# Optimization experiments

Measured on AMD Instinct MI355X. Metric: run time of the kernel, lower is better.

Reference implementation:

```python
import jax, jax.numpy as jnp
import numpy as np

N = 50000      # nodes
T = 24         # sequence length
D_IN = 16      # lstm input dim
H = 64         # lstm hidden dim
SD = 9         # static feature dim
G_IN, G_HID, G_OUT = 64, 64, 1
E = 1600000    # edges
NUM_GRAPHS = 500


def setup_inputs() -> dict:
    key = jax.random.key(0)
    ks = jax.random.split(key, 16)
    s = 0.1
    return {
        "x": jax.random.normal(ks[0], (N, T, D_IN), dtype=jnp.float32),
        "sdi": jax.random.normal(ks[1], (N, SD), dtype=jnp.float32),
        "edge_index": jax.random.randint(ks[2], (2, E), 0, N, dtype=jnp.int64),
        "batch": jnp.sort(jax.random.randint(ks[3], (N,), 0, NUM_GRAPHS, dtype=jnp.int64)),
        # LSTM params (torch gate order: i, f, g, o)
        "W_ih": s * jax.random.normal(ks[4], (4 * H, D_IN), dtype=jnp.float32),
        "W_hh": s * jax.random.normal(ks[5], (4 * H, H), dtype=jnp.float32),
        "b_ih": s * jax.random.normal(ks[6], (4 * H,), dtype=jnp.float32),
        "b_hh": s * jax.random.normal(ks[7], (4 * H,), dtype=jnp.float32),
        # Linear l1: (hidden + static) -> graph_input
        "l1_W": s * jax.random.normal(ks[8], (G_IN, H + SD), dtype=jnp.float32),
        "l1_b": s * jax.random.normal(ks[9], (G_IN,), dtype=jnp.float32),
        # GCNConv layers (weight stored [out, in] like torch Linear)
        "gcn1_W": s * jax.random.normal(ks[10], (G_HID, G_IN), dtype=jnp.float32),
        "gcn1_b": s * jax.random.normal(ks[11], (G_HID,), dtype=jnp.float32),
        "gcn2_W": s * jax.random.normal(ks[12], (G_OUT, G_HID), dtype=jnp.float32),
        "gcn2_b": s * jax.random.normal(ks[13], (G_OUT,), dtype=jnp.float32),
    }


def _lstm_last_hidden(x, W_ih, W_hh, b_ih, b_hh):
    # x: [N, T, D]; returns final hidden state h_T: [N, H]
    xg = jnp.einsum("ntd,gd->tng", x, W_ih) + (b_ih + b_hh)  # [T, N, 4H]
    h0 = jnp.zeros((x.shape[0], H), x.dtype)
    c0 = jnp.zeros((x.shape[0], H), x.dtype)

    def step(carry, g_t):
        h, c = carry
        g = g_t + h @ W_hh.T
        i, f, gg, o = jnp.split(g, 4, axis=-1)
        i = jax.nn.sigmoid(i)
        f = jax.nn.sigmoid(f)
        gg = jnp.tanh(gg)
        o = jax.nn.sigmoid(o)
        c = f * c + i * gg
        h = o * jnp.tanh(c)
        return (h, c), None

    (h, _), _ = jax.lax.scan(step, (h0, c0), xg)
    return h


def _gcn_conv(x, edge_index, W, b):
    # PyG GCNConv: add self-loops, symmetric normalization, scatter-add at dst.
    n = x.shape[0]
    loop = jnp.arange(n, dtype=edge_index.dtype)
    row = jnp.concatenate([edge_index[0], loop])  # src
    col = jnp.concatenate([edge_index[1], loop])  # dst
    deg = jax.ops.segment_sum(jnp.ones_like(col, dtype=x.dtype), col, num_segments=n)
    dis = jnp.where(deg > 0, jax.lax.rsqrt(jnp.maximum(deg, 1.0)), 0.0)
    norm = dis[row] * dis[col]                    # [E + N]
    h = x @ W.T                                   # [N, out]
    msg = h[row] * norm[:, None]                  # gather + scale
    out = jax.ops.segment_sum(msg, col, num_segments=n)
    return out + b


def reference(x, sdi, edge_index, batch, W_ih, W_hh, b_ih, b_hh,
              l1_W, l1_b, gcn1_W, gcn1_b, gcn2_W, gcn2_b):
    h = _lstm_last_hidden(x, W_ih, W_hh, b_ih, b_hh)       # [N, H]
    z = jnp.concatenate([h, sdi], axis=-1) @ l1_W.T + l1_b  # [N, G_IN]
    z = jax.nn.relu(_gcn_conv(z, edge_index, gcn1_W, gcn1_b))
    z = _gcn_conv(z, edge_index, gcn2_W, gcn2_b)            # [N, 1]
    # global mean pool over graph ids
    sums = jax.ops.segment_sum(z, batch, num_segments=NUM_GRAPHS)
    cnts = jax.ops.segment_sum(jnp.ones((z.shape[0],), z.dtype), batch, num_segments=NUM_GRAPHS)
    pooled = sums / jnp.maximum(cnts, 1.0)[:, None]         # [G, 1]
    return pooled.reshape(-1)
```

## Files before the change

### kernel.cpp

```cpp
#include <hip/hip_runtime.h>
#include <hip/hip_bf16.h>

#define N_NODES 50000
#define T_SEQ 24
#define D_IN 16
#define H_DIM 64
#define SD 9
#define E_EDGES 1600000
#define NUM_GRAPHS 500
#define NBLK 196

typedef _Float16 half8 __attribute__((ext_vector_type(8)));
typedef _Float16 half4 __attribute__((ext_vector_type(4)));
typedef float floatx4 __attribute__((ext_vector_type(4)));

__device__ __forceinline__ float fsig(float x) {
    return __fdividef(1.0f, 1.0f + __expf(-x));
}
__device__ __forceinline__ float ftanh(float x) {
    return 1.0f - __fdividef(2.0f, 1.0f + __expf(2.0f * x));
}

__global__ __launch_bounds__(256, 2) void lstm_mfma(
    const float* __restrict__ x,
    const float* __restrict__ W_ih, const float* __restrict__ W_hh,
    const float* __restrict__ b_ih, const float* __restrict__ b_hh,
    float* __restrict__ hout)
{
    __shared__ _Float16 smem[2048 + 24 * 16 * 16];
    _Float16* hb0 = smem;
    _Float16* hb1 = smem + 1024;
    _Float16* xbuf = smem + 2048;

    const int tid  = threadIdx.x;
    const int lane = tid & 63;
    const int w    = tid >> 6;
    const int lr   = lane & 15;
    const int lg   = lane >> 4;
    const int nbase = blockIdx.x * 16;

    half8 bw[4][3];
    float bias[4];
#pragma unroll
    for (int ct = 0; ct < 4; ct++) {
        const int r = ct * 64 + w * 16 + lr;
        bias[ct] = b_ih[r] + b_hh[r];
#pragma unroll
        for (int kt = 0; kt < 2; kt++) {
            const float* p = W_hh + r * 64 + kt * 32 + 8 * lg;
            half8 f;
#pragma unroll
            for (int e = 0; e < 8; e++) f[e] = (_Float16)p[e];
            bw[ct][kt] = f;
        }
        half8 f = {(_Float16)0, (_Float16)0, (_Float16)0, (_Float16)0,
                   (_Float16)0, (_Float16)0, (_Float16)0, (_Float16)0};
        if (lg < 2) {
            const float* p = W_ih + r * 16 + 8 * lg;
#pragma unroll
            for (int e = 0; e < 8; e++) f[e] = (_Float16)p[e];
        }
        bw[ct][2] = f;
    }

#pragma unroll
    for (int it = 0; it < 6; it++) {
        const int f4 = tid + it * 256;
        const int fi = f4 * 4;
        const int n  = fi / 384;
        const int rem = fi - n * 384;
        const int t  = rem >> 4;
        const int d  = rem & 15;
        const float4 v = *reinterpret_cast<const float4*>(
            x + (size_t)(nbase + n) * 384 + rem);
        half4 hv = {(_Float16)v.x, (_Float16)v.y, (_Float16)v.z, (_Float16)v.w};
        *reinterpret_cast<half4*>(&xbuf[t * 256 + n * 16 + d]) = hv;
    }
    if (tid < 128) { ((int*)hb0)[tid] = 0; ((int*)hb0)[tid + 128] = 0; ((int*)hb0)[tid + 256] = 0; ((int*)hb0)[tid + 384] = 0; }

    const int u = w * 16 + lr;
    int ra[2];
#pragma unroll
    for (int kt = 0; kt < 2; kt++)
        ra[kt] = lr * 64 + 8 * ((4 * kt + lg) ^ (lr & 7));
    int woff[4];
#pragma unroll
    for (int j = 0; j < 4; j++) {
        const int nj = 4 * lg + j;
        woff[j] = nj * 64 + (u & 7) + 8 * ((u >> 3) ^ (nj & 7));
    }
    const int xro = lr * 16 + 8 * (lg & 1);

    float c_reg[4];
#pragma unroll
    for (int j = 0; j < 4; j++) c_reg[j] = 0.0f;

    __syncthreads();

    auto step = [&](int tl, bool last, _Float16* hR, _Float16* hW) {
        floatx4 acc[4];
#pragma unroll
        for (int ct = 0; ct < 4; ct++) {
            floatx4 a = {bias[ct], bias[ct], bias[ct], bias[ct]};
            acc[ct] = a;
        }
        const half8 ax = *reinterpret_cast<const half8*>(&xbuf[tl * 256 + xro]);
        const half8 ah0 = *reinterpret_cast<const half8*>(&hR[ra[0]]);
        const half8 ah1 = *reinterpret_cast<const half8*>(&hR[ra[1]]);
#pragma unroll
        for (int ct = 0; ct < 4; ct++)
            acc[ct] = __builtin_amdgcn_mfma_f32_16x16x32_f16(ah0, bw[ct][0], acc[ct], 0, 0, 0);
#pragma unroll
        for (int ct = 0; ct < 4; ct++)
            acc[ct] = __builtin_amdgcn_mfma_f32_16x16x32_f16(ah1, bw[ct][1], acc[ct], 0, 0, 0);
#pragma unroll
        for (int ct = 0; ct < 4; ct++)
            acc[ct] = __builtin_amdgcn_mfma_f32_16x16x32_f16(ax, bw[ct][2], acc[ct], 0, 0, 0);

#pragma unroll
        for (int j = 0; j < 4; j++) {
            const float ig = fsig(acc[0][j]);
            const float fg = fsig(acc[1][j]);
            const float gg = ftanh(acc[2][j]);
            const float og = fsig(acc[3][j]);
            const float cv = fg * c_reg[j] + ig * gg;
            c_reg[j] = cv;
            const float hv = og * ftanh(cv);
            hW[woff[j]] = (_Float16)hv;
            if (last) {
                const int gn = nbase + 4 * lg + j;
                hout[(size_t)gn * H_DIM + u] = hv;
            }
        }
        __syncthreads();
    };

    for (int tb = 0; tb < 6; tb++) {
        const int t0 = tb * 4;
        step(t0 + 0, false, hb0, hb1);
        step(t0 + 1, false, hb1, hb0);
        step(t0 + 2, false, hb0, hb1);
        step(t0 + 3, tb == 5, hb1, hb0);
    }
}

__global__ void count_deg(const int* __restrict__ ei, int* __restrict__ cnt) {
    int e = blockIdx.x * 256 + threadIdx.x;
    if (e < E_EDGES) {
        int c = ei[E_EDGES + e];
        if ((unsigned)c < N_NODES) atomicAdd(&cnt[c], 1);
    }
}

__global__ __launch_bounds__(256) void scanA(const int* __restrict__ cnt,
                                             int* __restrict__ ptr,
                                             float* __restrict__ dis,
                                             int* __restrict__ bsum)
{
    __shared__ int wsum[4];
    const int tid = threadIdx.x, lane = tid & 63, wv = tid >> 6;
    const int i = blockIdx.x * 256 + tid;
    const int orig = (i < N_NODES) ? cnt[i] : 0;
    int v = orig;
#pragma unroll
    for (int d = 1; d < 64; d <<= 1) {
        int nb = __shfl_up(v, d, 64);
        if (lane >= d) v += nb;
    }
    if (lane == 63) wsum[wv] = v;
    __syncthreads();
    int woff = 0;
#pragma unroll
    for (int k = 0; k < 3; k++) if (k < wv) woff += wsum[k];
    if (i < N_NODES) {
        ptr[i] = woff + v - orig;
        dis[i] = rsqrtf((float)(orig + 1));
    }
    if (tid == 255) bsum[blockIdx.x] = woff + v;
}

__global__ __launch_bounds__(256) void scanB(const int* __restrict__ bsum,
                                             int* __restrict__ boff,
                                             int* __restrict__ ptr)
{
    __shared__ int wsum[4];
    const int tid = threadIdx.x, lane = tid & 63, wv = tid >> 6;
    const int orig = (tid < NBLK) ? bsum[tid] : 0;
    int v = orig;
#pragma unroll
    for (int d = 1; d < 64; d <<= 1) {
        int nb = __shfl_up(v, d, 64);
        if (lane >= d) v += nb;
    }
    if (lane == 63) wsum[wv] = v;
    __syncthreads();
    int woff = 0;
#pragma unroll
    for (int k = 0; k < 3; k++) if (k < wv) woff += wsum[k];
    if (tid < NBLK) boff[tid] = woff + v - orig;
    if (tid == 255) ptr[N_NODES] = woff + v;
}

__global__ __launch_bounds__(256) void scanC(int* __restrict__ ptr,
                                             const int* __restrict__ boff,
                                             int* __restrict__ cursor)
{
    const int i = blockIdx.x * 256 + threadIdx.x;
    if (i < N_NODES) {
        const int p = ptr[i] + boff[blockIdx.x];
        ptr[i] = p;
        cursor[i] = p;
    }
}

__global__ void fill_csr(const int* __restrict__ ei, int* __restrict__ cursor,
                         int* __restrict__ csr)
{
    int e = blockIdx.x * 256 + threadIdx.x;
    if (e < E_EDGES) {
        int r = ei[e];
        int c = ei[E_EDGES + e];
        if ((unsigned)r < N_NODES && (unsigned)c < N_NODES) {
            int slot = atomicAdd(&cursor[c], 1);
            csr[slot] = r;
        }
    }
}

__global__ void combine_w(const float* __restrict__ g1W, const float* __restrict__ l1W,
                          const float* __restrict__ l1b,
                          float* __restrict__ Wc, float* __restrict__ bc)
{
    int idx = blockIdx.x * 256 + threadIdx.x;
    int o = idx / 74, j = idx - o * 74;
    if (o >= 64) return;
    float acc = 0.0f;
    if (j < 73) {
#pragma unroll 8
        for (int k = 0; k < 64; k++) acc += g1W[o * 64 + k] * l1W[k * 73 + j];
        Wc[o * 73 + j] = acc;
    } else {
#pragma unroll 8
        for (int k = 0; k < 64; k++) acc += g1W[o * 64 + k] * l1b[k];
        bc[o] = acc;
    }
}

__global__ __launch_bounds__(256) void xform1(
    const float* __restrict__ h, const float* __restrict__ sdi,
    const float* __restrict__ Wc, const float* __restrict__ bc,
    const float* __restrict__ dis, float* __restrict__ m)
{
    __shared__ float wlds[64 * 73];
    __shared__ float blds[64];
    __shared__ float row[4][80];
    for (int i = threadIdx.x; i < 64 * 73; i += 256) wlds[i] = Wc[i];
    if (threadIdx.x < 64) blds[threadIdx.x] = bc[threadIdx.x];
    __syncthreads();
    const int wv = threadIdx.x >> 6, o = threadIdx.x & 63;
    for (int n = blockIdx.x * 4 + wv; n < N_NODES; n += gridDim.x * 4) {
        row[wv][o] = h[(size_t)n * 64 + o];
        if (o < SD) row[wv][64 + o] = sdi[(size_t)n * SD + o];
        __builtin_amdgcn_wave_barrier();
        float acc = blds[o];
#pragma unroll 8
        for (int j = 0; j < 73; j++) acc += wlds[o * 73 + j] * row[wv][j];
        __builtin_amdgcn_wave_barrier();
        m[(size_t)n * 64 + o] = acc * dis[n];
    }
}

__global__ __launch_bounds__(256) void gatherfin1s2(
    const int* __restrict__ ptr, const int* __restrict__ csr,
    const float* __restrict__ m, const float* __restrict__ dis,
    const float* __restrict__ b1, const float* __restrict__ W2,
    float* __restrict__ s2)
{
    const int wid = (blockIdx.x * 256 + threadIdx.x) >> 6;
    const int f = threadIdx.x & 63;
    if (wid >= N_NODES) return;
    const int b = ptr[wid];
    const int e = ptr[wid + 1];
    float a0 = 0.0f, a1 = 0.0f, a2 = 0.0f, a3 = 0.0f;
    int i = b;
    for (; i + 4 <= e; i += 4) {
        const int s0 = csr[i], s1 = csr[i + 1], sc2 = csr[i + 2], s3 = csr[i + 3];
        a0 += m[(size_t)s0 * 64 + f];
        a1 += m[(size_t)s1 * 64 + f];
        a2 += m[(size_t)sc2 * 64 + f];
        a3 += m[(size_t)s3 * 64 + f];
    }
    for (; i < e; i++) a0 += m[(size_t)csr[i] * 64 + f];
    const float self = m[(size_t)wid * 64 + f];
    const float dn = dis[wid];
    const float v = dn * (((a0 + a1) + (a2 + a3)) + self) + b1[f];
    const float z1 = v > 0.0f ? v : 0.0f;
    float p = z1 * W2[f];
#pragma unroll
    for (int off = 32; off >= 1; off >>= 1) p += __shfl_xor(p, off, 64);
    if (f == 0) s2[wid] = dn * p;
}

__global__ void gather2fin(const int* __restrict__ ptr, const int* __restrict__ csr,
                           const float* __restrict__ s2, const float* __restrict__ dis,
                           const float* __restrict__ b2, const int* __restrict__ batch,
                           float* __restrict__ gsum, float* __restrict__ gcnt)
{
    int n = blockIdx.x * 256 + threadIdx.x;
    if (n >= N_NODES) return;
    const int b = ptr[n];
    const int e = ptr[n + 1];
    float a0 = 0.0f, a1 = 0.0f, a2 = 0.0f, a3 = 0.0f;
    int i = b;
    for (; i + 4 <= e; i += 4) {
        a0 += s2[csr[i]];
        a1 += s2[csr[i + 1]];
        a2 += s2[csr[i + 2]];
        a3 += s2[csr[i + 3]];
    }
    for (; i < e; i++) a0 += s2[csr[i]];
    const float z2 = dis[n] * (((a0 + a1) + (a2 + a3)) + s2[n]) + b2[0];
    const int g = batch[n];
    if ((unsigned)g < NUM_GRAPHS) {
        atomicAdd(&gsum[g], z2);
        atomicAdd(&gcnt[g], 1.0f);
    }
}

__global__ void pooldiv(const float* __restrict__ gsum, const float* __restrict__ gcnt,
                        float* __restrict__ out)
{
    int g = blockIdx.x * 256 + threadIdx.x;
    if (g < NUM_GRAPHS) out[g] = gsum[g] / fmaxf(gcnt[g], 1.0f);
}

extern "C" void kernel_launch(void* const* d_in, const int* in_sizes, int n_in,
                              void* d_out, int out_size, void* d_ws, size_t ws_size,
                              hipStream_t stream)
{
    const float* x     = (const float*)d_in[0];
    const float* sdi   = (const float*)d_in[1];
    const int*   ei    = (const int*)d_in[2];
    const int*   batch = (const int*)d_in[3];
    const float* W_ih  = (const float*)d_in[4];
    const float* W_hh  = (const float*)d_in[5];
    const float* b_ih  = (const float*)d_in[6];
    const float* b_hh  = (const float*)d_in[7];
    const float* l1_W  = (const float*)d_in[8];
    const float* l1_b  = (const float*)d_in[9];
    const float* g1_W  = (const float*)d_in[10];
    const float* g1_b  = (const float*)d_in[11];
    const float* g2_W  = (const float*)d_in[12];
    const float* g2_b  = (const float*)d_in[13];
    float* out = (float*)d_out;

    float* ws   = (float*)d_ws;
    float* A    = ws;
    float* C    = ws + 6400000;
    float* dis  = ws + 9600000;
    float* s2   = dis + 50000;
    float* gsum = s2 + 50000;
    float* gcnt = gsum + 500;
    int* cnt    = (int*)(gcnt + 500);
    int* ptr    = cnt + 50000;
    int* cursor = ptr + 50001;
    int* csr    = cursor + 50000;
    float* Wc   = (float*)(csr + E_EDGES);
    float* bc   = Wc + 64 * 73;
    int* bsum   = (int*)(bc + 64);
    int* boff   = bsum + NBLK;

    const int featBlocks = (N_NODES * 64 + 255) / 256;
    const int edgeBlocks = (E_EDGES + 255) / 256;

    lstm_mfma<<<N_NODES / 16, 256, 0, stream>>>(x, W_ih, W_hh, b_ih, b_hh, A);

    hipMemsetAsync(cnt, 0, 50000 * sizeof(int), stream);
    hipMemsetAsync(gsum, 0, 1000 * sizeof(float), stream);
    count_deg<<<edgeBlocks, 256, 0, stream>>>(ei, cnt);
    scanA<<<NBLK, 256, 0, stream>>>(cnt, ptr, dis, bsum);
    scanB<<<1, 256, 0, stream>>>(bsum, boff, ptr);
    scanC<<<NBLK, 256, 0, stream>>>(ptr, boff, cursor);
    fill_csr<<<edgeBlocks, 256, 0, stream>>>(ei, cursor, csr);
    combine_w<<<(64 * 74 + 255) / 256, 256, 0, stream>>>(g1_W, l1_W, l1_b, Wc, bc);

    xform1<<<1024, 256, 0, stream>>>(A, sdi, Wc, bc, dis, C);

    gatherfin1s2<<<featBlocks, 256, 0, stream>>>(ptr, csr, C, dis, g1_b, g2_W, s2);

    gather2fin<<<NBLK, 256, 0, stream>>>(ptr, csr, s2, dis, g2_b, batch, gsum, gcnt);
    pooldiv<<<2, 256, 0, stream>>>(gsum, gcnt, out);
}
```

Baseline: 584.9 us.

## Fuse combined l1/gcn1 linear transform into LSTM kernel epilogue via MFMA

```diff
diff --git a/kernel.cpp b/kernel.cpp
--- a/kernel.cpp
+++ b/kernel.cpp
@@ -25,7 +25,9 @@
     const float* __restrict__ x,
     const float* __restrict__ W_ih, const float* __restrict__ W_hh,
     const float* __restrict__ b_ih, const float* __restrict__ b_hh,
-    float* __restrict__ hout)
+    const float* __restrict__ Wc, const float* __restrict__ bc,
+    const float* __restrict__ sdi, const float* __restrict__ dis,
+    float* __restrict__ m_out)
 {
     __shared__ _Float16 smem[2048 + 24 * 16 * 16];
     _Float16* hb0 = smem;
@@ -61,6 +63,28 @@
             for (int e = 0; e < 8; e++) f[e] = (_Float16)p[e];
         }
         bw[ct][2] = f;
+    }
+
+    half8 bwc[3];
+    {
+        const int fr = w * 16 + lr;
+#pragma unroll
+        for (int kt = 0; kt < 2; kt++) {
+            const float* p = Wc + fr * 73 + kt * 32 + 8 * lg;
+            half8 f;
+#pragma unroll
+            for (int e = 0; e < 8; e++) f[e] = (_Float16)p[e];
+            bwc[kt] = f;
+        }
+        half8 f = {(_Float16)0, (_Float16)0, (_Float16)0, (_Float16)0,
+                   (_Float16)0, (_Float16)0, (_Float16)0, (_Float16)0};
+#pragma unroll
+        for (int e = 0; e < 8; e++) {
+            const int k2 = 8 * lg + e;
+            if (k2 < 9) f[e] = (_Float16)Wc[fr * 73 + 64 + k2];
+            else if (k2 == 9) f[e] = (_Float16)bc[fr];
+        }
+        bwc[2] = f;
     }
 
 #pragma unroll
@@ -97,7 +121,7 @@
 
     __syncthreads();
 
-    auto step = [&](int tl, bool last, _Float16* hR, _Float16* hW) {
+    auto step = [&](int tl, _Float16* hR, _Float16* hW) {
         floatx4 acc[4];
 #pragma unroll
         for (int ct = 0; ct < 4; ct++) {
@@ -127,20 +151,36 @@
             c_reg[j] = cv;
             const float hv = og * ftanh(cv);
             hW[woff[j]] = (_Float16)hv;
-            if (last) {
-                const int gn = nbase + 4 * lg + j;
-                hout[(size_t)gn * H_DIM + u] = hv;
-            }
         }
         __syncthreads();
     };
 
     for (int tb = 0; tb < 6; tb++) {
         const int t0 = tb * 4;
-        step(t0 + 0, false, hb0, hb1);
-        step(t0 + 1, false, hb1, hb0);
-        step(t0 + 2, false, hb0, hb1);
-        step(t0 + 3, tb == 5, hb1, hb0);
+        step(t0 + 0, hb0, hb1);
+        step(t0 + 1, hb1, hb0);
+        step(t0 + 2, hb0, hb1);
+        step(t0 + 3, hb1, hb0);
+    }
+
+    half8 axs = {(_Float16)0, (_Float16)0, (_Float16)0, (_Float16)0,
+                 (_Float16)0, (_Float16)0, (_Float16)0, (_Float16)0};
+#pragma unroll
+    for (int e = 0; e < 8; e++) {
+        const int k2 = 8 * lg + e;
+        if (k2 < 9) axs[e] = (_Float16)sdi[(size_t)(nbase + lr) * SD + k2];
+        else if (k2 == 9) axs[e] = (_Float16)1.0f;
+    }
+    const half8 fh0 = *reinterpret_cast<const half8*>(&hb0[ra[0]]);
+    const half8 fh1 = *reinterpret_cast<const half8*>(&hb0[ra[1]]);
+    floatx4 am = {0.0f, 0.0f, 0.0f, 0.0f};
+    am = __builtin_amdgcn_mfma_f32_16x16x32_f16(fh0, bwc[0], am, 0, 0, 0);
+    am = __builtin_amdgcn_mfma_f32_16x16x32_f16(fh1, bwc[1], am, 0, 0, 0);
+    am = __builtin_amdgcn_mfma_f32_16x16x32_f16(axs, bwc[2], am, 0, 0, 0);
+#pragma unroll
+    for (int j = 0; j < 4; j++) {
+        const int gn = nbase + 4 * lg + j;
+        m_out[(size_t)gn * 64 + u] = am[j] * dis[gn];
     }
 }
 
@@ -243,30 +283,6 @@
 #pragma unroll 8
         for (int k = 0; k < 64; k++) acc += g1W[o * 64 + k] * l1b[k];
         bc[o] = acc;
-    }
-}
-
-__global__ __launch_bounds__(256) void xform1(
-    const float* __restrict__ h, const float* __restrict__ sdi,
-    const float* __restrict__ Wc, const float* __restrict__ bc,
-    const float* __restrict__ dis, float* __restrict__ m)
-{
-    __shared__ float wlds[64 * 73];
-    __shared__ float blds[64];
-    __shared__ float row[4][80];
-    for (int i = threadIdx.x; i < 64 * 73; i += 256) wlds[i] = Wc[i];
-    if (threadIdx.x < 64) blds[threadIdx.x] = bc[threadIdx.x];
-    __syncthreads();
-    const int wv = threadIdx.x >> 6, o = threadIdx.x & 63;
-    for (int n = blockIdx.x * 4 + wv; n < N_NODES; n += gridDim.x * 4) {
-        row[wv][o] = h[(size_t)n * 64 + o];
-        if (o < SD) row[wv][64 + o] = sdi[(size_t)n * SD + o];
-        __builtin_amdgcn_wave_barrier();
-        float acc = blds[o];
-#pragma unroll 8
-        for (int j = 0; j < 73; j++) acc += wlds[o * 73 + j] * row[wv][j];
-        __builtin_amdgcn_wave_barrier();
-        m[(size_t)n * 64 + o] = acc * dis[n];
     }
 }
 
@@ -355,7 +371,6 @@
     float* out = (float*)d_out;
 
     float* ws   = (float*)d_ws;
-    float* A    = ws;
     float* C    = ws + 6400000;
     float* dis  = ws + 9600000;
     float* s2   = dis + 50000;
@@ -373,8 +388,6 @@
     const int featBlocks = (N_NODES * 64 + 255) / 256;
     const int edgeBlocks = (E_EDGES + 255) / 256;
 
-    lstm_mfma<<<N_NODES / 16, 256, 0, stream>>>(x, W_ih, W_hh, b_ih, b_hh, A);
-
     hipMemsetAsync(cnt, 0, 50000 * sizeof(int), stream);
     hipMemsetAsync(gsum, 0, 1000 * sizeof(float), stream);
     count_deg<<<edgeBlocks, 256, 0, stream>>>(ei, cnt);
@@ -384,7 +397,8 @@
     fill_csr<<<edgeBlocks, 256, 0, stream>>>(ei, cursor, csr);
     combine_w<<<(64 * 74 + 255) / 256, 256, 0, stream>>>(g1_W, l1_W, l1_b, Wc, bc);
 
-    xform1<<<1024, 256, 0, stream>>>(A, sdi, Wc, bc, dis, C);
+    lstm_mfma<<<N_NODES / 16, 256, 0, stream>>>(x, W_ih, W_hh, b_ih, b_hh,
+                                                Wc, bc, sdi, dis, C);
 
     gatherfin1s2<<<featBlocks, 256, 0, stream>>>(ptr, csr, C, dis, g1_b, g2_W, s2);
 
```

Result: faster. 551.9 us (-5.7%).
